# Performance work log

Measured on AMD Instinct MI355X. Metric: run time of the kernel, lower is better.

The kernel has to match this reference:

```python
import jax, jax.numpy as jnp
import numpy as np

B, C, OC, K, HW = 32, 256, 256, 3, 56
M, G = 2, 2
GAP = max(16, C // 16)          # input_gap = 16
MO = M * OC                      # fc1 out channels = 512
FC2_OUT = OC * C * K * K         # 589824
PER = FC2_OUT // MO              # per-group out channels of fc2 = 1152


def setup_inputs() -> dict:
    key = jax.random.key(0)
    ks = jax.random.split(key, 6)
    x = jax.random.normal(ks[0], (B, C, HW, HW), dtype=jnp.float32)
    reduce_w = jax.random.normal(ks[1], (GAP, C), dtype=jnp.float32) / np.sqrt(C)
    reduce_b = jnp.zeros((GAP,), dtype=jnp.float32)
    fc1_w = jax.random.normal(ks[2], (MO, GAP), dtype=jnp.float32) / np.sqrt(GAP)
    # fc2: grouped 1x1 conv, groups=G*OC=512, 1 in-channel per group -> weight (FC2_OUT,)
    fc2_w = jax.random.normal(ks[3], (FC2_OUT,), dtype=jnp.float32)
    fc2_b = jax.random.normal(ks[4], (FC2_OUT,), dtype=jnp.float32) * 0.01
    return {"x": x, "reduce_w": reduce_w, "reduce_b": reduce_b,
            "fc1_w": fc1_w, "fc2_w": fc2_w, "fc2_b": fc2_b}


def reference(x, reduce_w, reduce_b, fc1_w, fc2_w, fc2_b):
    b, c, h, w = x.shape
    # global average pool -> (b, C)
    gap = x.mean(axis=(2, 3))
    # reduce: 1x1 conv on 1x1 map == linear
    g = gap @ reduce_w.T + reduce_b                      # (b, GAP)
    # fc1 (no bias) + sigmoid
    a = jax.nn.sigmoid(g @ fc1_w.T)                      # (b, MO)
    # fc2: grouped 1x1 conv with 1 input channel per group:
    # out[:, g*PER + j] = a[:, g] * fc2_w[g*PER + j] + fc2_b[g*PER + j]
    wk = a[:, :, None] * fc2_w.reshape(MO, PER)[None] + fc2_b.reshape(MO, PER)[None]
    wk = wk.reshape(b * OC, c, K, K)                     # per-sample conv kernels
    pad = K // 2
    y = jax.lax.conv_general_dilated(
        x.reshape(1, b * c, h, w), wk,
        window_strides=(1, 1), padding=[(pad, pad), (pad, pad)],
        feature_group_count=b,
        dimension_numbers=("NCHW", "OIHW", "NCHW"))
    return y.reshape(b, OC, y.shape[2], y.shape[3])
```

## Files before the change

### kernel.cpp

```cpp
#include <hip/hip_runtime.h>
#include <hip/hip_bf16.h>
#include <stdint.h>

#define NB   32
#define NC   256
#define NOC  256
#define HWD  56
#define NPIX 3136
#define PW   58
#define PPIX 3364
#define KTOT 2304
#define MOD  512
#define GAPD 16

#define XBT_BYTES ((size_t)NB * PPIX * NC * 2)
#define WA_BYTES  ((size_t)NB * NOC * KTOT * 2)

typedef __bf16 bf16x8 __attribute__((ext_vector_type(8)));
typedef float  f32x4  __attribute__((ext_vector_type(4)));
typedef unsigned short u16x8 __attribute__((ext_vector_type(8)));

__device__ __forceinline__ unsigned short f2bf(float f) {
    union { float f; unsigned int u; } v; v.f = f;
    unsigned int u = v.u;
    return (unsigned short)((u + 0x7FFFu + ((u >> 16) & 1u)) >> 16);
}

__global__ void wk_kernel(const float* __restrict__ gap,
                          const float* __restrict__ rw, const float* __restrict__ rb,
                          const float* __restrict__ f1w,
                          const float* __restrict__ f2w, const float* __restrict__ f2b,
                          unsigned short* __restrict__ wa) {
    __shared__ float sgap[NB * 257];
    __shared__ float srw[GAPD * 257];
    __shared__ float ssg[NB * GAPD];
    __shared__ float sa[2 * NB];
    __shared__ float sw[KTOT];
    __shared__ float sbv[KTOT];
    __shared__ unsigned short sx[9 * 264];
    int oc = blockIdx.x, c = threadIdx.x;
    #pragma unroll
    for (int i = 0; i < 32; ++i) {
        int idx = i * 256 + c;
        sgap[(idx >> 8) * 257 + (idx & 255)] = gap[idx];
    }
    #pragma unroll
    for (int i = 0; i < 16; ++i) {
        int idx = i * 256 + c;
        srw[(idx >> 8) * 257 + (idx & 255)] = rw[idx];
    }
    const float4* wsrc = (const float4*)(f2w + (size_t)oc * KTOT);
    const float4* bsrc = (const float4*)(f2b + (size_t)oc * KTOT);
    #pragma unroll
    for (int i = 0; i < 3; ++i) {
        int idx = i * 256 + c;
        if (idx < 576) {
            ((float4*)sw)[idx] = wsrc[idx];
            ((float4*)sbv)[idx] = bsrc[idx];
        }
    }
    __syncthreads();
    #pragma unroll
    for (int e = 0; e < 2; ++e) {
        int pair = c * 2 + e;
        int b = pair >> 4, tt = pair & 15;
        float s = rb[tt];
        for (int k = 0; k < NC; ++k) s += sgap[b * 257 + k] * srw[tt * 257 + k];
        ssg[b * GAPD + tt] = s;
    }
    __syncthreads();
    if (c < 64) {
        int b = c >> 1, e = c & 1;
        float s = 0.f;
        #pragma unroll
        for (int tt = 0; tt < GAPD; ++tt)
            s += ssg[b * GAPD + tt] * f1w[(2 * oc + e) * GAPD + tt];
        sa[c] = 1.0f / (1.0f + __expf(-s));
    }
    __syncthreads();
    float w9[9], b9[9];
    #pragma unroll
    for (int s = 0; s < 9; ++s) { w9[s] = sw[c * 9 + s]; b9[s] = sbv[c * 9 + s]; }
    const int hi = (c >= 128);
    const int rd1 = (c >> 5) * 528 + (c & 31) * 16;
    const int rd2 = 8 * 528 + c * 16;
    for (int b = 0; b < NB; ++b) {
        float a = hi ? sa[2 * b + 1] : sa[2 * b];
        #pragma unroll
        for (int s = 0; s < 9; ++s)
            sx[s * 264 + c] = f2bf(a * w9[s] + b9[s]);
        __syncthreads();
        unsigned short* dst = wa + (size_t)(b * NOC + oc) * KTOT;
        {
            u16x8 v = *(const u16x8*)((const char*)sx + rd1);
            *(u16x8*)(dst + (c >> 5) * 256 + (c & 31) * 8) = v;
        }
        if (c < 32) {
            u16x8 v = *(const u16x8*)((const char*)sx + rd2);
            *(u16x8*)(dst + 8 * 256 + c * 8) = v;
        }
        __syncthreads();
    }
}

#define TSTR 59
__global__ void xpose_kernel(const float* __restrict__ x, unsigned short* __restrict__ xbt,
                             float* __restrict__ gap) {
    __shared__ unsigned short tile[NC * TSTR];
    int py = blockIdx.x, b = blockIdx.y, t = threadIdx.x;
    int wv = t >> 6, l = t & 63;
    const u16x8 z = {};
    unsigned short* xb = xbt + (size_t)b * PPIX * NC;
    if (t < 64)
        *(u16x8*)(xb + ((size_t)(1 + py) * PW + ((t >= 32) ? 57 : 0)) * NC + (t & 31) * 8) = z;
    if (py == 0)
        for (int i = t; i < 1856; i += 256)
            *(u16x8*)(xb + (size_t)(i >> 5) * NC + (i & 31) * 8) = z;
    if (py == 55)
        for (int i = t; i < 1856; i += 256)
            *(u16x8*)(xb + (size_t)(57 * PW + (i >> 5)) * NC + (i & 31) * 8) = z;

    const float* xs = x + (size_t)b * NC * NPIX + py * HWD;
    int q = l & 15;
    int rb4 = l >> 4;
    #pragma unroll
    for (int it = 0; it < 16; ++it) {
        int c = wv * 64 + it * 4 + rb4;
        float4 v = {0.f, 0.f, 0.f, 0.f};
        if (q < 14) {
            v = *(const float4*)(xs + (size_t)c * NPIX + q * 4);
            unsigned short* tr = tile + c * TSTR + q * 4;
            tr[0] = f2bf(v.x); tr[1] = f2bf(v.y); tr[2] = f2bf(v.z); tr[3] = f2bf(v.w);
        }
        float s4 = v.x + v.y + v.z + v.w;
        s4 += __shfl_xor(s4, 1);
        s4 += __shfl_xor(s4, 2);
        s4 += __shfl_xor(s4, 4);
        s4 += __shfl_xor(s4, 8);
        if (q == 0) atomicAdd(&gap[b * NC + c], s4 * (1.0f / NPIX));
    }
    __syncthreads();
    int cch = t & 31, pg = t >> 5;
    for (int i = 0; i < 7; ++i) {
        int px = pg * 7 + i;
        u16x8 v;
        #pragma unroll
        for (int j = 0; j < 8; ++j) v[j] = tile[(cch * 8 + j) * TSTR + px];
        *(u16x8*)(xb + ((size_t)(1 + py) * PW + 1 + px) * NC + cch * 8) = v;
    }
}

#define SLICE 32768
#define BOFS  16384

#define PWAIT(N) do { asm volatile("s_waitcnt vmcnt(" #N ")" ::: "memory"); \
    __builtin_amdgcn_s_barrier(); __builtin_amdgcn_sched_barrier(0); } while (0)

__global__ __launch_bounds__(512, 2) void conv_gemm(
    const unsigned short* __restrict__ wa,
    const unsigned short* __restrict__ xbt,
    float* __restrict__ out)
{
    __shared__ __attribute__((aligned(16))) char lds[4 * SLICE];

    const int bid = blockIdx.x;
    const int wg  = (bid & 7) * 56 + (bid >> 3);
    const int b   = wg / 14, nt = wg % 14;

    const int t = threadIdx.x;
    const int w = t >> 6, l = t & 63;
    const int wm = w >> 1, wn = w & 1;

    const unsigned short* waB = wa + (size_t)b * NOC * KTOT;
    const unsigned short* xbB = xbt + (size_t)b * PPIX * NC;

    const unsigned short* srcA[2];
    const unsigned short* srcB[2];
    #pragma unroll
    for (int j = 0; j < 2; ++j) {
        int cix = j * 512 + t;
        int cc  = cix & 63;
        int row = (cix >> 6) * 16 + (cc >> 2);
        int qv  = (cc & 3) ^ ((cc >> 3) & 3);
        srcA[j] = waB + (size_t)row * KTOT + qv * 8;
        int pg = nt * 224 + row; if (pg > NPIX - 1) pg = NPIX - 1;
        int py = pg / 56, px = pg - py * 56;
        srcB[j] = xbB + (size_t)((py + 1) * PW + (px + 1)) * NC + qv * 8;
    }
    const int t16 = t * 16;

    auto issue = [&](int tp, int slot) {
        char* sb = lds + slot * SLICE;
        const int koff = tp * 32;
        const int s9 = tp >> 3;
        const int dy = (s9 >= 6) ? 2 : ((s9 >= 3) ? 1 : 0);
        const int dx = s9 - dy * 3;
        const int bsh = ((dy - 1) * PW + (dx - 1)) * NC + (tp & 7) * 32;
        #pragma unroll
        for (int j = 0; j < 2; ++j)
            __builtin_amdgcn_global_load_lds(
                (const __attribute__((address_space(1))) void*)(srcA[j] + koff),
                (__attribute__((address_space(3))) void*)(sb + j * 8192 + t16), 16, 0, 0);
        #pragma unroll
        for (int j = 0; j < 2; ++j)
            __builtin_amdgcn_global_load_lds(
                (const __attribute__((address_space(1))) void*)(srcB[j] + bsh),
                (__attribute__((address_space(3))) void*)(sb + BOFS + j * 8192 + t16), 16, 0, 0);
    };

    const int physq16 = (((l >> 4) ^ ((l >> 1) & 3)) << 4);
    const int arow = (l & 15) << 6;

    f32x4 acc[4][7] = {};

    auto compute = [&](int slot) {
        const char* sb = lds + slot * SLICE;
        bf16x8 af[4], bfr[7];
        #pragma unroll
        for (int m = 0; m < 4; ++m)
            af[m] = *(const bf16x8*)(sb + (wm * 4 + m) * 1024 + arow + physq16);
        #pragma unroll
        for (int j = 0; j < 7; ++j)
            bfr[j] = *(const bf16x8*)(sb + BOFS + (wn * 7 + j) * 1024 + arow + physq16);
        __builtin_amdgcn_s_setprio(1);
        #pragma unroll
        for (int m = 0; m < 4; ++m)
            #pragma unroll
            for (int j = 0; j < 7; ++j)
                acc[m][j] = __builtin_amdgcn_mfma_f32_16x16x32_bf16(af[m], bfr[j], acc[m][j], 0, 0, 0);
        __builtin_amdgcn_s_setprio(0);
    };

    issue(0, 0); issue(1, 1);

    #pragma unroll 4
    for (int p = 0; p < 70; ++p) {
        issue(p + 2, (p + 2) & 3);
        PWAIT(8);
        compute(p & 3);
    }
    PWAIT(4); compute(70 & 3);
    PWAIT(0); compute(71 & 3);

    const int ocb = wm * 64 + ((l >> 4) << 2);
    const int pxb = nt * 224 + wn * 112 + (l & 15);
    #pragma unroll
    for (int i = 0; i < 4; ++i) {
        #pragma unroll
        for (int j = 0; j < 7; ++j) {
            float* o = out + ((size_t)(b * NOC + ocb + i * 16)) * NPIX + pxb + j * 16;
            o[0]        = acc[i][j][0];
            o[NPIX]     = acc[i][j][1];
            o[2 * NPIX] = acc[i][j][2];
            o[3 * NPIX] = acc[i][j][3];
        }
    }
}

extern "C" void kernel_launch(void* const* d_in, const int* in_sizes, int n_in,
                              void* d_out, int out_size, void* d_ws, size_t ws_size,
                              hipStream_t stream) {
    (void)in_sizes; (void)n_in; (void)out_size; (void)ws_size;
    const float* x   = (const float*)d_in[0];
    const float* rw  = (const float*)d_in[1];
    const float* rb  = (const float*)d_in[2];
    const float* f1w = (const float*)d_in[3];
    const float* f2w = (const float*)d_in[4];
    const float* f2b = (const float*)d_in[5];
    float* out = (float*)d_out;

    char* wsb = (char*)d_ws;
    unsigned short* xbt = (unsigned short*)wsb;
    unsigned short* wa  = (unsigned short*)(wsb + XBT_BYTES);
    float* gap = (float*)(wsb + XBT_BYTES + WA_BYTES);

    hipMemsetAsync(gap, 0, (size_t)NB * NC * 4, stream);
    xpose_kernel<<<dim3(56, 32), 256, 0, stream>>>(x, xbt, gap);
    wk_kernel<<<dim3(256), 256, 0, stream>>>(gap, rw, rb, f1w, f2w, f2b, wa);
    conv_gemm<<<dim3(448), 512, 0, stream>>>(wa, xbt, out);
}
```

Before: 191.2 us.

## Stage padded input strip once per channel group and reuse across 3x3 taps

```diff
diff --git a/kernel.cpp b/kernel.cpp
--- a/kernel.cpp
+++ b/kernel.cpp
@@ -37,7 +37,6 @@
     __shared__ float sa[2 * NB];
     __shared__ float sw[KTOT];
     __shared__ float sbv[KTOT];
-    __shared__ unsigned short sx[9 * 264];
     int oc = blockIdx.x, c = threadIdx.x;
     #pragma unroll
     for (int i = 0; i < 32; ++i) {
@@ -82,24 +81,12 @@
     #pragma unroll
     for (int s = 0; s < 9; ++s) { w9[s] = sw[c * 9 + s]; b9[s] = sbv[c * 9 + s]; }
     const int hi = (c >= 128);
-    const int rd1 = (c >> 5) * 528 + (c & 31) * 16;
-    const int rd2 = 8 * 528 + c * 16;
     for (int b = 0; b < NB; ++b) {
         float a = hi ? sa[2 * b + 1] : sa[2 * b];
+        unsigned short* dst = wa + (size_t)(b * NOC + oc) * KTOT + (c >> 5) * 288 + (c & 31);
         #pragma unroll
         for (int s = 0; s < 9; ++s)
-            sx[s * 264 + c] = f2bf(a * w9[s] + b9[s]);
-        __syncthreads();
-        unsigned short* dst = wa + (size_t)(b * NOC + oc) * KTOT;
-        {
-            u16x8 v = *(const u16x8*)((const char*)sx + rd1);
-            *(u16x8*)(dst + (c >> 5) * 256 + (c & 31) * 8) = v;
-        }
-        if (c < 32) {
-            u16x8 v = *(const u16x8*)((const char*)sx + rd2);
-            *(u16x8*)(dst + 8 * 256 + c * 8) = v;
-        }
-        __syncthreads();
+            dst[s * 32] = f2bf(a * w9[s] + b9[s]);
     }
 }
 
@@ -150,18 +137,20 @@
     }
 }
 
-#define SLICE 32768
-#define BOFS  16384
-
-#define PWAIT(N) do { asm volatile("s_waitcnt vmcnt(" #N ")" ::: "memory"); \
+#define A_SLOT   16384
+#define STRIP_OFF 65536
+#define STRIP_SZ  24576
+
+#define PWAIT_(N) do { asm volatile("s_waitcnt vmcnt(" #N ")" ::: "memory"); \
     __builtin_amdgcn_s_barrier(); __builtin_amdgcn_sched_barrier(0); } while (0)
+#define PWAIT(N) PWAIT_(N)
 
 __global__ __launch_bounds__(512, 2) void conv_gemm(
     const unsigned short* __restrict__ wa,
     const unsigned short* __restrict__ xbt,
     float* __restrict__ out)
 {
-    __shared__ __attribute__((aligned(16))) char lds[4 * SLICE];
+    __shared__ __attribute__((aligned(16))) char lds[STRIP_OFF + 3 * STRIP_SZ];
 
     const int bid = blockIdx.x;
     const int wg  = (bid & 7) * 56 + (bid >> 3);
@@ -173,9 +162,9 @@
 
     const unsigned short* waB = wa + (size_t)b * NOC * KTOT;
     const unsigned short* xbB = xbt + (size_t)b * PPIX * NC;
+    const int py0 = nt * 4;
 
     const unsigned short* srcA[2];
-    const unsigned short* srcB[2];
     #pragma unroll
     for (int j = 0; j < 2; ++j) {
         int cix = j * 512 + t;
@@ -183,45 +172,58 @@
         int row = (cix >> 6) * 16 + (cc >> 2);
         int qv  = (cc & 3) ^ ((cc >> 3) & 3);
         srcA[j] = waB + (size_t)row * KTOT + qv * 8;
-        int pg = nt * 224 + row; if (pg > NPIX - 1) pg = NPIX - 1;
-        int py = pg / 56, px = pg - py * 56;
-        srcB[j] = xbB + (size_t)((py + 1) * PW + (px + 1)) * NC + qv * 8;
+    }
+    const unsigned short* srcS[3];
+    #pragma unroll
+    for (int j = 0; j < 3; ++j) {
+        int g = j * 512 + t;
+        int sp = g >> 2; if (sp > 347) sp = 347;
+        int kq = ((g & 3) - (sp >> 1)) & 3;
+        srcS[j] = xbB + (size_t)(py0 * 58 + sp) * NC + kq * 8;
     }
     const int t16 = t * 16;
 
-    auto issue = [&](int tp, int slot) {
-        char* sb = lds + slot * SLICE;
-        const int koff = tp * 32;
-        const int s9 = tp >> 3;
-        const int dy = (s9 >= 6) ? 2 : ((s9 >= 3) ? 1 : 0);
-        const int dx = s9 - dy * 3;
-        const int bsh = ((dy - 1) * PW + (dx - 1)) * NC + (tp & 7) * 32;
+    auto stageA = [&](int tp, int slot) {
+        char* sb = lds + slot * A_SLOT;
         #pragma unroll
         for (int j = 0; j < 2; ++j)
             __builtin_amdgcn_global_load_lds(
-                (const __attribute__((address_space(1))) void*)(srcA[j] + koff),
+                (const __attribute__((address_space(1))) void*)(srcA[j] + tp * 32),
                 (__attribute__((address_space(3))) void*)(sb + j * 8192 + t16), 16, 0, 0);
-        #pragma unroll
-        for (int j = 0; j < 2; ++j)
+    };
+    auto stageS = [&](int cg, int buf) {
+        char* sb = lds + STRIP_OFF + buf * STRIP_SZ;
+        #pragma unroll
+        for (int j = 0; j < 3; ++j)
             __builtin_amdgcn_global_load_lds(
-                (const __attribute__((address_space(1))) void*)(srcB[j] + bsh),
-                (__attribute__((address_space(3))) void*)(sb + BOFS + j * 8192 + t16), 16, 0, 0);
+                (const __attribute__((address_space(1))) void*)(srcS[j] + cg * 32),
+                (__attribute__((address_space(3))) void*)(sb + j * 8192 + t16), 16, 0, 0);
     };
 
     const int physq16 = (((l >> 4) ^ ((l >> 1) & 3)) << 4);
     const int arow = (l & 15) << 6;
+    const int kq = l >> 4;
+    int rs[7];
+    #pragma unroll
+    for (int j = 0; j < 7; ++j) {
+        int prow = wn * 112 + j * 16 + (l & 15);
+        rs[j] = prow + 2 * (prow / 56);
+    }
 
     f32x4 acc[4][7] = {};
 
-    auto compute = [&](int slot) {
-        const char* sb = lds + slot * SLICE;
+    auto compute = [&](int aslot, int buf, int sh) {
+        const char* ab = lds + aslot * A_SLOT;
+        const char* sb = lds + STRIP_OFF + buf * STRIP_SZ;
         bf16x8 af[4], bfr[7];
         #pragma unroll
         for (int m = 0; m < 4; ++m)
-            af[m] = *(const bf16x8*)(sb + (wm * 4 + m) * 1024 + arow + physq16);
-        #pragma unroll
-        for (int j = 0; j < 7; ++j)
-            bfr[j] = *(const bf16x8*)(sb + BOFS + (wn * 7 + j) * 1024 + arow + physq16);
+            af[m] = *(const bf16x8*)(ab + (wm * 4 + m) * 1024 + arow + physq16);
+        #pragma unroll
+        for (int j = 0; j < 7; ++j) {
+            int sp = rs[j] + sh;
+            bfr[j] = *(const bf16x8*)(sb + sp * 64 + (((kq + (sp >> 1)) & 3) << 4));
+        }
         __builtin_amdgcn_s_setprio(1);
         #pragma unroll
         for (int m = 0; m < 4; ++m)
@@ -231,16 +233,36 @@
         __builtin_amdgcn_s_setprio(0);
     };
 
-    issue(0, 0); issue(1, 1);
-
-    #pragma unroll 4
-    for (int p = 0; p < 70; ++p) {
-        issue(p + 2, (p + 2) & 3);
-        PWAIT(8);
-        compute(p & 3);
-    }
-    PWAIT(4); compute(70 & 3);
-    PWAIT(0); compute(71 & 3);
+#define STEP(P, VM, DOSTRIP, CG, SH)                      \
+    do {                                                  \
+        if ((P) + 2 < 72) stageA((P) + 2, ((P) + 2) & 3); \
+        PWAIT(VM);                                        \
+        if (DOSTRIP) stageS((CG) + 2, ((CG) + 2) % 3);    \
+        compute((P) & 3, (CG) % 3, SH);                   \
+    } while (0)
+
+    stageS(0, 0); stageS(1, 1); stageA(0, 0); stageA(1, 1);
+
+    #pragma unroll 1
+    for (int cg = 0; cg < 6; ++cg) {
+        const int p0 = cg * 9;
+        STEP(p0 + 0, 4, 1, cg, 0);
+        STEP(p0 + 1, 7, 0, cg, 1);
+        STEP(p0 + 2, 7, 0, cg, 2);
+        STEP(p0 + 3, 4, 0, cg, 58);
+        STEP(p0 + 4, 4, 0, cg, 59);
+        STEP(p0 + 5, 4, 0, cg, 60);
+        STEP(p0 + 6, 4, 0, cg, 116);
+        STEP(p0 + 7, 4, 0, cg, 117);
+        STEP(p0 + 8, 4, 0, cg, 118);
+    }
+    STEP(54, 4, 0, 6, 0);   STEP(55, 4, 0, 6, 1);   STEP(56, 4, 0, 6, 2);
+    STEP(57, 4, 0, 6, 58);  STEP(58, 4, 0, 6, 59);  STEP(59, 4, 0, 6, 60);
+    STEP(60, 4, 0, 6, 116); STEP(61, 4, 0, 6, 117); STEP(62, 4, 0, 6, 118);
+    STEP(63, 4, 0, 7, 0);   STEP(64, 4, 0, 7, 1);   STEP(65, 4, 0, 7, 2);
+    STEP(66, 4, 0, 7, 58);  STEP(67, 4, 0, 7, 59);  STEP(68, 4, 0, 7, 60);
+    STEP(69, 4, 0, 7, 116); STEP(70, 2, 0, 7, 117); STEP(71, 0, 0, 7, 118);
+#undef STEP
 
     const int ocb = wm * 64 + ((l >> 4) << 2);
     const int pxb = nt * 224 + wn * 112 + (l & 15);
```

Result: slower. 282.0 us (+47.5%).
